# Kernel tuning notes

Measured on AMD Instinct MI355X. Metric: run time of the kernel, lower is better.

The kernel has to match this reference:

```python
import jax, jax.numpy as jnp
import numpy as np

WINDOW_SIZES = (5, 10, 20)
EPS = 1e-5


def setup_inputs() -> dict:
    key = jax.random.key(0)
    x = jax.random.normal(key, (32, 4096, 128), dtype=jnp.float32)
    weights = jnp.ones((len(WINDOW_SIZES),), dtype=jnp.float32)
    return {"x": x, "weights": weights}


def _sliding_center_norm(x, w, eps):
    # x: (B, L, F). Normalize each length-w window (biased var), keep only the
    # center element of each window, then zero-pad back to length L.
    B, L, F = x.shape
    c = w // 2
    n = L - w + 1  # number of windows
    zp = jnp.zeros((B, 1, F), x.dtype)
    cs = jnp.concatenate([zp, jnp.cumsum(x, axis=1)], axis=1)        # (B, L+1, F)
    cs2 = jnp.concatenate([zp, jnp.cumsum(x * x, axis=1)], axis=1)   # (B, L+1, F)
    mean = (cs[:, w:] - cs[:, :n]) / w                                # (B, n, F)
    m2 = (cs2[:, w:] - cs2[:, :n]) / w
    var = jnp.maximum(m2 - mean * mean, 0.0)  # biased var (unbiased=False)
    std = jnp.sqrt(var + eps)
    center = x[:, c:c + n]  # element at center index of each window
    normed = (center - mean) / std
    pad_right = L - n - c
    return jnp.pad(normed, ((0, 0), (c, pad_right), (0, 0)))


def reference(x, weights):
    x = jnp.nan_to_num(x, nan=0.0, posinf=0.0, neginf=0.0)
    w_soft = jax.nn.softmax(weights, axis=0)
    out = jnp.zeros_like(x)
    for i, w in enumerate(WINDOW_SIZES):
        out = out + w_soft[i] * _sliding_center_norm(x, w, EPS)
    return out
```

## Files before the change

kernel.cpp:

```cpp
#include <hip/hip_runtime.h>
#include <math.h>

#pragma clang fp contract(off)

#define LL 4096
#define FF 128
#define NB 32
#define BASE 16
#define NBLK 256
#define NOB 16

__device__ __forceinline__ float sani(float v) {
    return (fabsf(v) <= 3.0e38f) ? v : 0.0f;
}

__global__ __launch_bounds__(256) void k_tiles(const float* __restrict__ x,
                                               float2* __restrict__ T0) {
    __shared__ float xs[32 * FF];
    const int bid  = blockIdx.x;
    const int pair = bid & 127;
    const int b    = bid >> 7;
    const int tid  = (int)threadIdx.x;
    const float* xb = x + ((size_t)b * LL + (size_t)pair * 32) * FF;
    for (int i = tid; i < 32 * FF; i += 256) xs[i] = sani(xb[i]);
    __syncthreads();
    const int f = tid & 127, t = tid >> 7;
    const int blk = pair * 2 + t;
    float cs, cs2;
    {
        const float v = xs[(t * 16) * FF + f];
        cs = v; cs2 = __fmul_rn(v, v);
    }
#pragma unroll
    for (int u = 1; u < 16; ++u) {
        const float v = xs[(t * 16 + u) * FF + f];
        cs  = __fadd_rn(cs,  v);
        cs2 = __fadd_rn(cs2, __fmul_rn(v, v));
    }
    T0[((size_t)b * NBLK + blk) * FF + f] = make_float2(cs, cs2);
}

__global__ __launch_bounds__(64) void k_prefix(const float2* __restrict__ T0,
                                               float2* __restrict__ P) {
    const int bid = blockIdx.x;
    const int fh = bid & 1, b = bid >> 1;
    const int f  = fh * 64 + (int)threadIdx.x;
    const float2* t0c = T0 + (size_t)b * NBLK * FF + f;
    float2*       pc  = P  + (size_t)b * NBLK * FF + f;
    pc[0] = make_float2(0.0f, 0.0f);
    float S2x = 0.0f, S2y = 0.0f;
    for (int g = 0; g < NOB; ++g) {
        float s1x = 0.0f, s1y = 0.0f;
#pragma unroll
        for (int i = 0; i < 16; ++i) {
            const int B = g * 16 + i;
            const float2 t = t0c[(size_t)B * FF];
            if (i == 0) { s1x = t.x; s1y = t.y; }
            else        { s1x = __fadd_rn(s1x, t.x); s1y = __fadd_rn(s1y, t.y); }
            if (B < NBLK - 1) {
                float px = s1x, py = s1y;
                if (g > 0) { px = __fadd_rn(s1x, S2x); py = __fadd_rn(s1y, S2y); }
                pc[(size_t)(B + 1) * FF] = make_float2(px, py);
            }
        }
        if (g == 0) { S2x = s1x; S2y = s1y; }
        else        { S2x = __fadd_rn(S2x, s1x); S2y = __fadd_rn(S2y, s1y); }
    }
}

template<bool GUARD>
__global__ __launch_bounds__(256) void k_win_reg(const float* __restrict__ x,
                                                 const float* __restrict__ w,
                                                 const float2* __restrict__ P,
                                                 float* __restrict__ out,
                                                 int pair_base, int pair_stride) {
    const int pair = pair_base + (int)blockIdx.x * pair_stride;
    const int b    = (int)blockIdx.y;
    const int tid  = (int)threadIdx.x;
    const int f    = tid & 127;
    const int tile = pair * 2 + (tid >> 7);
    const int lbase = tile * 16;
    const int base  = lbase - 16;

    const float2* Pb = P + (size_t)b * NBLK * FF + f;
    float2 Pm = make_float2(0.0f, 0.0f), Pl = make_float2(0.0f, 0.0f);
    if (!GUARD || tile >= 1)        Pm = Pb[(size_t)(tile - 1) * FF];
    const float2 Pc = Pb[(size_t)tile * FF];
    if (!GUARD || tile <= NBLK - 2) Pl = Pb[(size_t)(tile + 1) * FF];

    const float* xb = x + ((size_t)b * LL + lbase) * FF + f;

    float Vx[48], Vy[48], xr[16];

#define SEG(OFF, PP)                                                          \
    {                                                                         \
        float cs = 0.0f, cs2 = 0.0f;                                          \
        _Pragma("unroll")                                                     \
        for (int u = 0; u < 16; ++u) {                                        \
            const int p = (OFF) + u;                                          \
            float v = 0.0f;                                                   \
            if (!GUARD || ((unsigned)(base + p) < (unsigned)LL))              \
                v = sani(xb[(size_t)(p - 16) * FF]);                          \
            if ((OFF) == 16) xr[u] = v;                                       \
            if (u == 0) { cs = v; cs2 = __fmul_rn(v, v); }                    \
            else { cs = __fadd_rn(cs, v);                                     \
                   cs2 = __fadd_rn(cs2, __fmul_rn(v, v)); }                   \
            Vx[p] = __fadd_rn(cs,  (PP).x);                                   \
            Vy[p] = __fadd_rn(cs2, (PP).y);                                   \
        }                                                                     \
    }
    SEG(0, Pm)
    SEG(16, Pc)
    SEG(32, Pl)
#undef SEG

    const float w0 = w[0], w1 = w[1], w2 = w[2];
    const float mx = fmaxf(w0, fmaxf(w1, w2));
    const float e0 = expf(w0 - mx), e1 = expf(w1 - mx), e2 = expf(w2 - mx);
    const float s  = e0 + e1 + e2;
    const float ws0 = e0 / s, ws1 = e1 / s, ws2 = e2 / s;

    float* ob = out + ((size_t)b * LL + lbase) * FF + f;

#pragma unroll
    for (int u = 0; u < 16; ++u) {
        const int l = lbase + u;
        const float xc = xr[u];
        const float g5  = (l >= 2  && l <= LL - 3)  ? ws0 : 0.0f;
        const float g10 = (l >= 5  && l <= LL - 5)  ? ws1 : 0.0f;
        const float g20 = (l >= 10 && l <= LL - 10) ? ws2 : 0.0f;
        float o;
        {
            const float mean = (Vx[u + 18] - Vx[u + 13]) * 0.2f;
            const float m2   = (Vy[u + 18] - Vy[u + 13]) * 0.2f;
            const float var  = fmaxf(m2 - mean * mean, 0.0f);
            o = g5 * ((xc - mean) * rsqrtf(var + 1e-5f));
        }
        {
            const float mean = (Vx[u + 20] - Vx[u + 10]) * 0.1f;
            const float m2   = (Vy[u + 20] - Vy[u + 10]) * 0.1f;
            const float var  = fmaxf(m2 - mean * mean, 0.0f);
            o += g10 * ((xc - mean) * rsqrtf(var + 1e-5f));
        }
        {
            const float mean = (Vx[u + 25] - Vx[u + 5]) * 0.05f;
            const float m2   = (Vy[u + 25] - Vy[u + 5]) * 0.05f;
            const float var  = fmaxf(m2 - mean * mean, 0.0f);
            o += g20 * ((xc - mean) * rsqrtf(var + 1e-5f));
        }
        ob[(size_t)u * FF] = o;
    }
}

__global__ __launch_bounds__(256) void fan_blocked(const float* __restrict__ x,
                                                   const float* __restrict__ w,
                                                   float* __restrict__ out) {
    __shared__ float2 V[LL];
    __shared__ float2 T0s[NBLK];
    __shared__ float2 T1[NOB];
    __shared__ float2 S2[NOB];
    const int col = blockIdx.x;
    const int f   = col & (FF - 1);
    const int b   = col >> 7;
    const int tid = (int)threadIdx.x;
    const float* xcol = x   + (size_t)b * LL * FF + f;
    float*       ocol = out + (size_t)b * LL * FF + f;
    for (int l = tid; l < LL; l += 256) {
        const float v = sani(xcol[(size_t)l * FF]);
        V[l] = make_float2(v, __fmul_rn(v, v));
    }
    __syncthreads();
    {
        const int bse = tid * BASE;
        float cs = V[bse].x, cs2 = V[bse].y;
        for (int u = 1; u < BASE; ++u) {
            const float2 e = V[bse + u];
            cs = __fadd_rn(cs, e.x); cs2 = __fadd_rn(cs2, e.y);
            V[bse + u] = make_float2(cs, cs2);
        }
        T0s[tid] = make_float2(cs, cs2);
    }
    __syncthreads();
    if (tid < NOB) {
        const int bse = tid * BASE;
        float cs = T0s[bse].x, cs2 = T0s[bse].y;
        for (int u = 1; u < BASE; ++u) {
            const float2 e = T0s[bse + u];
            cs = __fadd_rn(cs, e.x); cs2 = __fadd_rn(cs2, e.y);
            T0s[bse + u] = make_float2(cs, cs2);
        }
        T1[tid] = make_float2(cs, cs2);
    }
    __syncthreads();
    if (tid == 0) {
        float cs = T1[0].x, cs2 = T1[0].y;
        S2[0] = T1[0];
        for (int o = 1; o < NOB; ++o) {
            cs = __fadd_rn(cs, T1[o].x); cs2 = __fadd_rn(cs2, T1[o].y);
            S2[o] = make_float2(cs, cs2);
        }
    }
    __syncthreads();
    {
        const int blk = tid;
        if (blk > 0) {
            const int B = blk - 1, ob2 = B >> 4;
            float2 Pp = T0s[B];
            if (ob2 > 0) {
                const float2 s2 = S2[ob2 - 1];
                Pp = make_float2(__fadd_rn(Pp.x, s2.x), __fadd_rn(Pp.y, s2.y));
            }
            const int bse = blk * BASE;
            for (int u = 0; u < BASE; ++u) {
                const float2 sv = V[bse + u];
                V[bse + u] = make_float2(__fadd_rn(sv.x, Pp.x), __fadd_rn(sv.y, Pp.y));
            }
        }
    }
    __syncthreads();
    const float w0 = w[0], w1 = w[1], w2 = w[2];
    const float mx = fmaxf(w0, fmaxf(w1, w2));
    const float e0 = expf(w0 - mx), e1 = expf(w1 - mx), e2 = expf(w2 - mx);
    const float s  = e0 + e1 + e2;
    const float ws0 = e0 / s, ws1 = e1 / s, ws2 = e2 / s;
    auto PV = [&](int j) -> float2 {
        if (j <= 0) return make_float2(0.0f, 0.0f);
        int idx = j - 1; if (idx > LL - 1) idx = LL - 1;
        return V[idx];
    };
    for (int l = tid; l < LL; l += 256) {
        const float xc = sani(xcol[(size_t)l * FF]);
        const float2 A5 = PV(l + 3), B5 = PV(l - 2);
        const float2 A10 = PV(l + 5), B10 = PV(l - 5);
        const float2 A20 = PV(l + 10), B20 = PV(l - 10);
        const float g5  = (l >= 2  && l <= LL - 3)  ? ws0 : 0.0f;
        const float g10 = (l >= 5  && l <= LL - 5)  ? ws1 : 0.0f;
        const float g20 = (l >= 10 && l <= LL - 10) ? ws2 : 0.0f;
        float o;
        {
            const float mean = (A5.x - B5.x) * 0.2f;
            const float m2   = (A5.y - B5.y) * 0.2f;
            const float var  = fmaxf(m2 - mean * mean, 0.0f);
            o = g5 * ((xc - mean) * rsqrtf(var + 1e-5f));
        }
        {
            const float mean = (A10.x - B10.x) * 0.1f;
            const float m2   = (A10.y - B10.y) * 0.1f;
            const float var  = fmaxf(m2 - mean * mean, 0.0f);
            o += g10 * ((xc - mean) * rsqrtf(var + 1e-5f));
        }
        {
            const float mean = (A20.x - B20.x) * 0.05f;
            const float m2   = (A20.y - B20.y) * 0.05f;
            const float var  = fmaxf(m2 - mean * mean, 0.0f);
            o += g20 * ((xc - mean) * rsqrtf(var + 1e-5f));
        }
        ocol[(size_t)l * FF] = o;
    }
}

extern "C" void kernel_launch(void* const* d_in, const int* in_sizes, int n_in,
                              void* d_out, int out_size, void* d_ws, size_t ws_size,
                              hipStream_t stream) {
    const float* x = (const float*)d_in[0];
    const float* w = (const float*)d_in[1];
    float* out     = (float*)d_out;

    const size_t t0_bytes = (size_t)NB * NBLK * FF * sizeof(float2);
    if (ws_size >= 2 * t0_bytes) {
        float2* T0 = (float2*)d_ws;
        float2* P  = (float2*)((char*)d_ws + t0_bytes);
        k_tiles <<<dim3(NB * 128), dim3(256), 0, stream>>>(x, T0);
        k_prefix<<<dim3(NB * 2),   dim3(64),  0, stream>>>(T0, P);
        k_win_reg<false><<<dim3(126, NB), dim3(256), 0, stream>>>(x, w, P, out, 1, 1);
        k_win_reg<true ><<<dim3(2,   NB), dim3(256), 0, stream>>>(x, w, P, out, 0, 127);
    } else {
        fan_blocked<<<dim3(NB * FF), dim3(256), 0, stream>>>(x, w, out);
    }
}
```

Before: 80.60 us.

## Split serial prefix into parallel two-level scan and stage window tiles in LDS

The single serial per-column prefix kernel, which ran only 64 blocks, is replaced by two kernels. One does an in-place scan of 16-tile groups across 512 blocks, and the other scans the group totals. The window kernel now rebuilds the needed prefix values from the two levels. It stages a 64-row slab of x in shared memory with float4 loads instead of strided per-thread global loads, and it drops the separate guarded boundary launch. The tile-sum kernel also no longer goes through shared memory. This adds one kernel launch, some extra prefix loads per thread and 32 KB of LDS per block, which may lower occupancy.

Result: faster. 64.70 us (-19.7%).

```diff
diff --git a/kernel.cpp b/kernel.cpp
--- a/kernel.cpp
+++ b/kernel.cpp
@@ -16,102 +16,125 @@
 
 __global__ __launch_bounds__(256) void k_tiles(const float* __restrict__ x,
                                                float2* __restrict__ T0) {
-    __shared__ float xs[32 * FF];
-    const int bid  = blockIdx.x;
-    const int pair = bid & 127;
-    const int b    = bid >> 7;
-    const int tid  = (int)threadIdx.x;
-    const float* xb = x + ((size_t)b * LL + (size_t)pair * 32) * FF;
-    for (int i = tid; i < 32 * FF; i += 256) xs[i] = sani(xb[i]);
-    __syncthreads();
-    const int f = tid & 127, t = tid >> 7;
-    const int blk = pair * 2 + t;
-    float cs, cs2;
-    {
-        const float v = xs[(t * 16) * FF + f];
-        cs = v; cs2 = __fmul_rn(v, v);
-    }
-#pragma unroll
-    for (int u = 1; u < 16; ++u) {
-        const float v = xs[(t * 16 + u) * FF + f];
-        cs  = __fadd_rn(cs,  v);
-        cs2 = __fadd_rn(cs2, __fmul_rn(v, v));
-    }
-    T0[((size_t)b * NBLK + blk) * FF + f] = make_float2(cs, cs2);
-}
-
-__global__ __launch_bounds__(64) void k_prefix(const float2* __restrict__ T0,
-                                               float2* __restrict__ P) {
-    const int bid = blockIdx.x;
-    const int fh = bid & 1, b = bid >> 1;
-    const int f  = fh * 64 + (int)threadIdx.x;
-    const float2* t0c = T0 + (size_t)b * NBLK * FF + f;
-    float2*       pc  = P  + (size_t)b * NBLK * FF + f;
-    pc[0] = make_float2(0.0f, 0.0f);
-    float S2x = 0.0f, S2y = 0.0f;
-    for (int g = 0; g < NOB; ++g) {
-        float s1x = 0.0f, s1y = 0.0f;
-#pragma unroll
-        for (int i = 0; i < 16; ++i) {
-            const int B = g * 16 + i;
-            const float2 t = t0c[(size_t)B * FF];
-            if (i == 0) { s1x = t.x; s1y = t.y; }
-            else        { s1x = __fadd_rn(s1x, t.x); s1y = __fadd_rn(s1y, t.y); }
-            if (B < NBLK - 1) {
-                float px = s1x, py = s1y;
-                if (g > 0) { px = __fadd_rn(s1x, S2x); py = __fadd_rn(s1y, S2y); }
-                pc[(size_t)(B + 1) * FF] = make_float2(px, py);
-            }
-        }
-        if (g == 0) { S2x = s1x; S2y = s1y; }
-        else        { S2x = __fadd_rn(S2x, s1x); S2y = __fadd_rn(S2y, s1y); }
-    }
-}
-
-template<bool GUARD>
-__global__ __launch_bounds__(256) void k_win_reg(const float* __restrict__ x,
-                                                 const float* __restrict__ w,
-                                                 const float2* __restrict__ P,
-                                                 float* __restrict__ out,
-                                                 int pair_base, int pair_stride) {
-    const int pair = pair_base + (int)blockIdx.x * pair_stride;
+    const int pair = (int)blockIdx.x;
     const int b    = (int)blockIdx.y;
     const int tid  = (int)threadIdx.x;
     const int f    = tid & 127;
     const int tile = pair * 2 + (tid >> 7);
-    const int lbase = tile * 16;
-    const int base  = lbase - 16;
-
-    const float2* Pb = P + (size_t)b * NBLK * FF + f;
-    float2 Pm = make_float2(0.0f, 0.0f), Pl = make_float2(0.0f, 0.0f);
-    if (!GUARD || tile >= 1)        Pm = Pb[(size_t)(tile - 1) * FF];
-    const float2 Pc = Pb[(size_t)tile * FF];
-    if (!GUARD || tile <= NBLK - 2) Pl = Pb[(size_t)(tile + 1) * FF];
-
-    const float* xb = x + ((size_t)b * LL + lbase) * FF + f;
-
-    float Vx[48], Vy[48], xr[16];
-
-#define SEG(OFF, PP)                                                          \
-    {                                                                         \
-        float cs = 0.0f, cs2 = 0.0f;                                          \
-        _Pragma("unroll")                                                     \
-        for (int u = 0; u < 16; ++u) {                                        \
-            const int p = (OFF) + u;                                          \
-            float v = 0.0f;                                                   \
-            if (!GUARD || ((unsigned)(base + p) < (unsigned)LL))              \
-                v = sani(xb[(size_t)(p - 16) * FF]);                          \
-            if ((OFF) == 16) xr[u] = v;                                       \
-            if (u == 0) { cs = v; cs2 = __fmul_rn(v, v); }                    \
-            else { cs = __fadd_rn(cs, v);                                     \
-                   cs2 = __fadd_rn(cs2, __fmul_rn(v, v)); }                   \
-            Vx[p] = __fadd_rn(cs,  (PP).x);                                   \
-            Vy[p] = __fadd_rn(cs2, (PP).y);                                   \
-        }                                                                     \
-    }
-    SEG(0, Pm)
-    SEG(16, Pc)
-    SEG(32, Pl)
+    const float* xb = x + ((size_t)b * LL + (size_t)tile * 16) * FF + f;
+    float cs, cs2;
+    {
+        const float v = sani(xb[0]);
+        cs = v; cs2 = __fmul_rn(v, v);
+    }
+#pragma unroll
+    for (int u = 1; u < 16; ++u) {
+        const float v = sani(xb[(size_t)u * FF]);
+        cs  = __fadd_rn(cs,  v);
+        cs2 = __fadd_rn(cs2, __fmul_rn(v, v));
+    }
+    T0[((size_t)b * NBLK + tile) * FF + f] = make_float2(cs, cs2);
+}
+
+__global__ __launch_bounds__(128) void k_pref_a(float2* __restrict__ T0) {
+    const int g = (int)blockIdx.x & 15;
+    const int b = (int)blockIdx.x >> 4;
+    const int f = (int)threadIdx.x;
+    float2* p = T0 + ((size_t)b * NBLK + (size_t)g * 16) * FF + f;
+    float2 t[16];
+#pragma unroll
+    for (int i = 0; i < 16; ++i) t[i] = p[(size_t)i * FF];
+    float sx = t[0].x, sy = t[0].y;
+#pragma unroll
+    for (int i = 1; i < 16; ++i) {
+        sx = __fadd_rn(sx, t[i].x);
+        sy = __fadd_rn(sy, t[i].y);
+        p[(size_t)i * FF] = make_float2(sx, sy);
+    }
+}
+
+__global__ __launch_bounds__(128) void k_pref_b(const float2* __restrict__ S1,
+                                                float2* __restrict__ S2) {
+    const int b = (int)blockIdx.x;
+    const int f = (int)threadIdx.x;
+    const float2* base = S1 + (size_t)b * NBLK * FF + f;
+    float2* s2 = S2 + (size_t)b * NOB * FF + f;
+    float2 t = base[(size_t)15 * FF];
+    float sx = t.x, sy = t.y;
+    s2[0] = t;
+    for (int g = 1; g < NOB; ++g) {
+        const float2 tg = base[(size_t)(g * 16 + 15) * FF];
+        sx = __fadd_rn(sx, tg.x);
+        sy = __fadd_rn(sy, tg.y);
+        s2[(size_t)g * FF] = make_float2(sx, sy);
+    }
+}
+
+__global__ __launch_bounds__(256) void k_win2(const float* __restrict__ x,
+                                              const float* __restrict__ w,
+                                              const float2* __restrict__ S1,
+                                              const float2* __restrict__ S2,
+                                              float* __restrict__ out) {
+    __shared__ float xs[64 * FF];
+    const int pair = (int)blockIdx.x;
+    const int b    = (int)blockIdx.y;
+    const int tid  = (int)threadIdx.x;
+    const int l0   = pair * 32 - 16;
+
+    const float* xb = x + (size_t)b * LL * FF;
+#pragma unroll
+    for (int it = 0; it < 8; ++it) {
+        const int idx = it * 1024 + tid * 4;
+        const int row = idx >> 7;
+        const int col = idx & 127;
+        const int g   = l0 + row;
+        float4 v = make_float4(0.0f, 0.0f, 0.0f, 0.0f);
+        if ((unsigned)g < (unsigned)LL)
+            v = *reinterpret_cast<const float4*>(xb + (size_t)g * FF + col);
+        v.x = sani(v.x); v.y = sani(v.y); v.z = sani(v.z); v.w = sani(v.w);
+        *reinterpret_cast<float4*>(&xs[row * FF + col]) = v;
+    }
+    __syncthreads();
+
+    const int t    = tid >> 7;
+    const int f    = tid & 127;
+    const int tile = pair * 2 + t;
+    const int rb   = t * 16;
+
+    auto PB = [&](int B) -> float2 {
+        if (B < 0) return make_float2(0.0f, 0.0f);
+        float2 p = S1[((size_t)b * NBLK + B) * FF + f];
+        const int g = B >> 4;
+        if (g > 0) {
+            const float2 s2 = S2[((size_t)b * NOB + (g - 1)) * FF + f];
+            p.x = __fadd_rn(p.x, s2.x);
+            p.y = __fadd_rn(p.y, s2.y);
+        }
+        return p;
+    };
+    const float2 PA  = PB(tile - 2);
+    const float2 PBm = PB(tile - 1);
+    const float2 PC  = PB(tile);
+
+    float Vx[41], Vy[41], xr[16];
+
+#define SEG(P0, N, PP, SAVE)                                         \
+    {                                                                \
+        float cs = 0.0f, cs2 = 0.0f;                                 \
+        _Pragma("unroll")                                            \
+        for (int u = 0; u < (N); ++u) {                              \
+            const float v = xs[(rb + (P0) + u) * FF + f];            \
+            if (SAVE) xr[u] = v;                                     \
+            if (u == 0) { cs = v; cs2 = __fmul_rn(v, v); }           \
+            else { cs = __fadd_rn(cs, v);                            \
+                   cs2 = __fadd_rn(cs2, __fmul_rn(v, v)); }          \
+            Vx[(P0) + u] = __fadd_rn(cs,  (PP).x);                   \
+            Vy[(P0) + u] = __fadd_rn(cs2, (PP).y);                   \
+        }                                                            \
+    }
+    SEG(0,  16, PA,  false)
+    SEG(16, 16, PBm, true)
+    SEG(32, 9,  PC,  false)
 #undef SEG
 
     const float w0 = w[0], w1 = w[1], w2 = w[2];
@@ -120,11 +143,11 @@
     const float s  = e0 + e1 + e2;
     const float ws0 = e0 / s, ws1 = e1 / s, ws2 = e2 / s;
 
-    float* ob = out + ((size_t)b * LL + lbase) * FF + f;
+    float* ob = out + ((size_t)b * LL + (size_t)tile * 16) * FF + f;
 
 #pragma unroll
     for (int u = 0; u < 16; ++u) {
-        const int l = lbase + u;
+        const int l = tile * 16 + u;
         const float xc = xr[u];
         const float g5  = (l >= 2  && l <= LL - 3)  ? ws0 : 0.0f;
         const float g10 = (l >= 5  && l <= LL - 5)  ? ws1 : 0.0f;
@@ -269,11 +292,11 @@
     const size_t t0_bytes = (size_t)NB * NBLK * FF * sizeof(float2);
     if (ws_size >= 2 * t0_bytes) {
         float2* T0 = (float2*)d_ws;
-        float2* P  = (float2*)((char*)d_ws + t0_bytes);
-        k_tiles <<<dim3(NB * 128), dim3(256), 0, stream>>>(x, T0);
-        k_prefix<<<dim3(NB * 2),   dim3(64),  0, stream>>>(T0, P);
-        k_win_reg<false><<<dim3(126, NB), dim3(256), 0, stream>>>(x, w, P, out, 1, 1);
-        k_win_reg<true ><<<dim3(2,   NB), dim3(256), 0, stream>>>(x, w, P, out, 0, 127);
+        float2* S2 = (float2*)((char*)d_ws + t0_bytes);
+        k_tiles <<<dim3(128, NB), dim3(256), 0, stream>>>(x, T0);
+        k_pref_a<<<dim3(NB * 16), dim3(128), 0, stream>>>(T0);
+        k_pref_b<<<dim3(NB),      dim3(128), 0, stream>>>(T0, S2);
+        k_win2  <<<dim3(128, NB), dim3(256), 0, stream>>>(x, w, T0, S2, out);
     } else {
         fan_blocked<<<dim3(NB * FF), dim3(256), 0, stream>>>(x, w, out);
     }
```
